# Optimization experiments

Measured on AMD Instinct MI355X. Metric: run time of the kernel, lower is better.

The kernel has to match this reference:

```python
import jax, jax.numpy as jnp
import numpy as np

B, T, IN, H, OUT = 512, 2048, 32, 256, 1
DT = 0.1
EPS = 1e-5


def setup_inputs() -> dict:
    key = jax.random.key(0)
    ks = jax.random.split(key, 16)
    n = lambda k, s, sc: jax.random.normal(k, s, jnp.float32) * sc
    d = {}
    d["x"] = n(ks[0], (B, T, IN), 1.0)
    d["Win0"] = n(ks[1], (IN, H), IN ** -0.5); d["bin0"] = jnp.zeros(H, jnp.float32)
    d["Wrec0"] = n(ks[2], (H, H), H ** -0.5); d["brec0"] = jnp.zeros(H, jnp.float32)
    d["Wattn0"] = n(ks[3], (H, H), H ** -0.5); d["battn0"] = jnp.zeros(H, jnp.float32)
    d["Wev0"] = n(ks[4], (2 * IN, 1), (2 * IN) ** -0.5); d["bev0"] = jnp.zeros(1, jnp.float32)
    d["tau0"] = jnp.ones(H, jnp.float32)
    d["gamma0"] = jnp.ones(H, jnp.float32); d["beta0"] = jnp.zeros(H, jnp.float32)
    d["Win1"] = n(ks[5], (H, H), H ** -0.5); d["bin1"] = jnp.zeros(H, jnp.float32)
    d["Wrec1"] = n(ks[6], (H, H), H ** -0.5); d["brec1"] = jnp.zeros(H, jnp.float32)
    d["Wattn1"] = n(ks[7], (H, H), H ** -0.5); d["battn1"] = jnp.zeros(H, jnp.float32)
    d["Wev1"] = n(ks[8], (2 * H, 1), (2 * H) ** -0.5); d["bev1"] = jnp.zeros(1, jnp.float32)
    d["tau1"] = jnp.ones(H, jnp.float32)
    d["gamma1"] = jnp.ones(H, jnp.float32); d["beta1"] = jnp.zeros(H, jnp.float32)
    d["Wskip"] = n(ks[9], (H, H), H ** -0.5); d["bskip"] = jnp.zeros(H, jnp.float32)
    d["Wout"] = n(ks[10], (H, OUT), H ** -0.5); d["bout"] = jnp.zeros(OUT, jnp.float32)
    return d


def _cell(xt, h, prev, mask, Win, bin_, Wrec, brec, Wattn, battn, Wev, bev, tau):
    # event weight from current and previous (detached) input; masked to 0 at t==0
    ew = jax.nn.sigmoid(jnp.concatenate([xt, prev], axis=1) @ Wev + bev) * mask  # [B,1]
    inp = jnp.tanh(xt @ Win + bin_)
    attn = jax.nn.sigmoid(h @ Wattn + battn)
    rec = jnp.tanh((h * attn) @ Wrec + brec)
    tau_c = jnp.clip(tau, 0.1, 10.0)
    new_h = h + DT * ((-h + inp + rec) / tau_c) * (1.0 + ew)
    return new_h, ew


def _ln(h, g, b):
    mu = h.mean(-1, keepdims=True)
    v = ((h - mu) ** 2).mean(-1, keepdims=True)
    return (h - mu) * jax.lax.rsqrt(v + EPS) * g + b


def _forward(x, Win0, bin0, Wrec0, brec0, Wattn0, battn0, Wev0, bev0, tau0, gamma0, beta0,
             Win1, bin1, Wrec1, brec1, Wattn1, battn1, Wev1, bev1, tau1, gamma1, beta1,
             Wskip, bskip, Wout, bout):
    Bv, Tv, _ = x.shape

    def step(carry, xs):
        h0, h1, p0, p1 = carry
        xt, mask = xs  # xt [B,IN], mask scalar-ish [1,1]
        h0n, ew0 = _cell(xt, h0, p0, mask, Win0, bin0, Wrec0, brec0, Wattn0, battn0, Wev0, bev0, tau0)
        h0n = _ln(h0n, gamma0, beta0)
        # layer 1 consumes the freshly updated layer-0 hidden (matches inner-loop order)
        h1n, ew1 = _cell(h0n, h1, p1, mask, Win1, bin1, Wrec1, brec1, Wattn1, battn1, Wev1, bev1, tau1)
        h1n = _ln(h1n, gamma1, beta1) + h0n @ Wskip + bskip
        new_carry = (h0n, h1n, jax.lax.stop_gradient(xt), jax.lax.stop_gradient(h0n))
        return new_carry, (ew0[:, 0], ew1[:, 0])

    xT = jnp.swapaxes(x, 0, 1)  # [T,B,IN]
    mask = (jnp.arange(Tv) > 0).astype(x.dtype)[:, None, None]  # [T,1,1]
    init = (jnp.zeros((Bv, H), x.dtype), jnp.zeros((Bv, H), x.dtype),
            jnp.zeros((Bv, x.shape[-1]), x.dtype), jnp.zeros((Bv, H), x.dtype))
    (h0, h1, _, _), (ew0s, ew1s) = jax.lax.scan(step, init, (xT, mask))
    out = h1 @ Wout + bout  # [B,OUT]
    return out, jnp.swapaxes(ew0s, 0, 1), jnp.swapaxes(ew1s, 0, 1)  # event weights [B,T]


def reference(x, Win0, bin0, Wrec0, brec0, Wattn0, battn0, Wev0, bev0, tau0, gamma0, beta0,
              Win1, bin1, Wrec1, brec1, Wattn1, battn1, Wev1, bev1, tau1, gamma1, beta1,
              Wskip, bskip, Wout, bout):
    return _forward(x, Win0, bin0, Wrec0, brec0, Wattn0, battn0, Wev0, bev0, tau0, gamma0, beta0,
                    Win1, bin1, Wrec1, brec1, Wattn1, battn1, Wev1, bev1, tau1, gamma1, beta1,
                    Wskip, bskip, Wout, bout)
```

## Files before the change

kernel.cpp:

```cpp
#include <hip/hip_runtime.h>
#include <math.h>

#define Bsz 512
#define Tsz 2048
#define INsz 32
#define Hsz 256

typedef __attribute__((ext_vector_type(8))) _Float16 half8;
typedef __attribute__((ext_vector_type(4))) float f32x4;

__device__ __forceinline__ f32x4 mfma16h(half8 a, half8 b, f32x4 c) {
    return __builtin_amdgcn_mfma_f32_16x16x32_f16(a, b, c, 0, 0, 0);
}
__device__ __forceinline__ float fsigmoid(float x) { return 1.0f / (1.0f + __expf(-x)); }
__device__ __forceinline__ float ftanh(float x) {
    float e = __expf(-2.0f * fabsf(x));
    float r = (1.0f - e) / (1.0f + e);
    return copysignf(r, x);
}

__global__ void ew0k(const float* __restrict__ x, const float* __restrict__ Wev0,
                     const float* __restrict__ bev0, float* __restrict__ ew0p) {
    int idx = blockIdx.x * 256 + threadIdx.x;
    int t = idx & (Tsz - 1);
    float e = 0.0f;
    if (t > 0) {
        const float* xc = x + (size_t)idx * INsz;
        const float* xp = xc - INsz;
        float acc = bev0[0];
#pragma unroll
        for (int k = 0; k < INsz; ++k) acc += xc[k] * Wev0[k] + xp[k] * Wev0[INsz + k];
        e = fsigmoid(acc);
    }
    ew0p[idx] = e;
}

__global__ void prep_frag(const float* __restrict__ W, _Float16* __restrict__ dst, int KC) {
    int tile = blockIdx.x / KC, kc = blockIdx.x % KC;
    int lane = threadIdx.x;
    int n16 = lane & 15, q = lane >> 4;
#pragma unroll
    for (int j = 0; j < 8; ++j) {
        int k = kc * 32 + q * 8 + j;
        float wv = W[(size_t)k * Hsz + tile * 16 + n16];
        _Float16 hi = (_Float16)wv;
        _Float16 lo = (_Float16)(wv - (float)hi);
        size_t rec = ((size_t)tile * KC + kc) * 2;
        dst[(rec + 0) * 512 + lane * 8 + j] = hi;
        dst[(rec + 1) * 512 + lane * 8 + j] = lo;
    }
}

__global__ __launch_bounds__(512, 2) void fused(
    const float* __restrict__ x, const float* __restrict__ ew0p, float* __restrict__ ew1p,
    const _Float16* __restrict__ fA0, const _Float16* __restrict__ fR0, const _Float16* __restrict__ fI0,
    const _Float16* __restrict__ fA1, const _Float16* __restrict__ fR1,
    const _Float16* __restrict__ fI1, const _Float16* __restrict__ fS1,
    const float* __restrict__ bin0, const float* __restrict__ brec0, const float* __restrict__ battn0,
    const float* __restrict__ tau0, const float* __restrict__ gamma0, const float* __restrict__ beta0,
    const float* __restrict__ bin1, const float* __restrict__ brec1, const float* __restrict__ battn1,
    const float* __restrict__ tau1, const float* __restrict__ gamma1, const float* __restrict__ beta1,
    const float* __restrict__ bskip, const float* __restrict__ Wev1, const float* __restrict__ bev1,
    _Float16* __restrict__ h0nA, _Float16* __restrict__ h0nB,
    float* __restrict__ in1bA, float* __restrict__ in1bB,
    float* __restrict__ skpbA, float* __restrict__ skpbB,
    float* __restrict__ h1s, int C, int L, int nch) {

    __shared__ _Float16 sAh[4096], sAl[4096];
    __shared__ _Float16 sW[65536];
    __shared__ float red[16][8][2];

    const int tid = threadIdx.x;
    const int w = tid >> 6, lane = tid & 63;
    const int n16 = lane & 15, q = lane >> 4;
    const int bx = blockIdx.x;

    if (bx < 32) {
        const int ci = L;
        if (ci >= nch) return;
        _Float16* __restrict__ h0n = (ci & 1) ? h0nB : h0nA;
        const _Float16* __restrict__ h0prev = (ci & 1) ? h0nA : h0nB;
        const int t0 = ci * C;
        const int rb = bx;
        const int r0 = rb * 16;
        const int c0 = w * 16 + n16, c1 = c0 + 128;

        for (int i = tid; i < 8192; i += 512) {
            int rec = i >> 6, off = i & 63;
            ((int4*)sW)[i] = ((const int4*)(fA0 + (size_t)rec * 2 * 512))[off];
        }
        half8 rB[2][8][2];
#pragma unroll
        for (int t2 = 0; t2 < 2; ++t2) {
            const int tile = t2 ? w + 8 : w;
#pragma unroll
            for (int kc = 0; kc < 8; ++kc) {
#pragma unroll
                for (int sp = 0; sp < 2; ++sp)
                    rB[t2][kc][sp] = *(const half8*)(fR0 + (((size_t)tile * 8 + kc) * 2 + sp) * 512 + lane * 8);
            }
        }
        half8 iB[2][2];
#pragma unroll
        for (int t2 = 0; t2 < 2; ++t2) {
            const int tile = t2 ? w + 8 : w;
#pragma unroll
            for (int sp = 0; sp < 2; ++sp)
                iB[t2][sp] = *(const half8*)(fI0 + ((size_t)tile * 2 + sp) * 512 + lane * 8);
        }
        float cbi[2], cbr[2], cba[2], ctau[2], cg[2], cb[2];
#pragma unroll
        for (int t2 = 0; t2 < 2; ++t2) {
            const int col = t2 ? c1 : c0;
            cbi[t2] = bin0[col]; cbr[t2] = brec0[col]; cba[t2] = battn0[col];
            ctau[t2] = 0.1f / fminf(fmaxf(tau0[col], 0.1f), 10.0f);
            cg[t2] = gamma0[col]; cb[t2] = beta0[col];
        }
        {
            const int4* src = (const int4*)(h0prev + ((size_t)C * 32 + rb) * 8192);
            int4 vh = src[tid], vl = src[tid + 512];
            ((int4*)sAh)[tid] = vh; ((int4*)sAl)[tid] = vl;
            int4* dst0 = (int4*)(h0n + (size_t)rb * 8192);
            dst0[tid] = vh; dst0[tid + 512] = vl;
        }
        __syncthreads();
        float h0reg[2][4];
#pragma unroll
        for (int t2 = 0; t2 < 2; ++t2) {
            const int col = t2 ? c1 : c0;
#pragma unroll
            for (int r = 0; r < 4; ++r) {
                int idx = ((col >> 3) * 16 + (q * 4 + r)) * 8 + (col & 7);
                h0reg[t2][r] = (float)sAh[idx] + (float)sAl[idx];
            }
        }
        auto pw = [&](int row, int col, float v) {
            int idx = ((col >> 3) * 16 + row) * 8 + (col & 7);
            _Float16 h = (_Float16)v;
            sAh[idx] = h;
            sAl[idx] = (_Float16)(v - (float)h);
        };

        const float* xbase = x + (size_t)(r0 + n16) * Tsz * INsz;
        const _Float16* lo0 = fA0 + ((size_t)w * 8 * 2 + 1) * 512 + lane * 8;
        const _Float16* lo1 = fA0 + (((size_t)(w + 8) * 8) * 2 + 1) * 512 + lane * 8;

        float4 xv0 = *(const float4*)(xbase + (size_t)t0 * INsz + q * 8);
        float4 xv1 = *(const float4*)(xbase + (size_t)t0 * INsz + q * 8 + 4);

#pragma unroll 1
        for (int s = 0; s < C; ++s) {
            const int t = t0 + s;
            float e0r[4];
#pragma unroll
            for (int r = 0; r < 4; ++r)
                e0r[r] = ew0p[(size_t)(r0 + q * 4 + r) * Tsz + t];
            half8 xh, xl;
            {
                float xv[8] = {xv0.x, xv0.y, xv0.z, xv0.w, xv1.x, xv1.y, xv1.z, xv1.w};
#pragma unroll
                for (int j = 0; j < 8; ++j) {
                    _Float16 h = (_Float16)xv[j];
                    xh[j] = h;
                    xl[j] = (_Float16)(xv[j] - (float)h);
                }
            }
            if (s + 1 < C) {
                const float* xp = xbase + (size_t)(t + 1) * INsz + q * 8;
                xv0 = *(const float4*)xp;
                xv1 = *(const float4*)(xp + 4);
            }
            f32x4 aA0 = {0,0,0,0}, aA1 = {0,0,0,0};
            {
                half8 nl0 = *(const half8*)(lo0);
                half8 nl1 = *(const half8*)(lo1);
#pragma unroll
                for (int kc = 0; kc < 8; ++kc) {
                    half8 cl0 = nl0, cl1 = nl1;
                    if (kc < 7) {
                        nl0 = *(const half8*)(lo0 + (size_t)(kc + 1) * 2 * 512);
                        nl1 = *(const half8*)(lo1 + (size_t)(kc + 1) * 2 * 512);
                    }
                    half8 ah = *(const half8*)&sAh[((kc * 4 + q) * 16 + n16) * 8];
                    half8 al = *(const half8*)&sAl[((kc * 4 + q) * 16 + n16) * 8];
                    half8 bh0 = *(const half8*)&sW[((w * 8 + kc) * 512) + lane * 8];
                    half8 bh1 = *(const half8*)&sW[(((w + 8) * 8 + kc) * 512) + lane * 8];
                    aA0 = mfma16h(ah, bh0, aA0); aA1 = mfma16h(ah, bh1, aA1);
                    aA0 = mfma16h(al, bh0, aA0); aA1 = mfma16h(al, bh1, aA1);
                    aA0 = mfma16h(ah, cl0, aA0); aA1 = mfma16h(ah, cl1, aA1);
                    aA0 = mfma16h(al, cl0, aA0); aA1 = mfma16h(al, cl1, aA1);
                }
            }
            f32x4 aI0 = {0,0,0,0}, aI1 = {0,0,0,0};
            aI0 = mfma16h(xh, iB[0][0], aI0); aI1 = mfma16h(xh, iB[1][0], aI1);
            aI0 = mfma16h(xl, iB[0][0], aI0); aI1 = mfma16h(xl, iB[1][0], aI1);
            aI0 = mfma16h(xh, iB[0][1], aI0); aI1 = mfma16h(xh, iB[1][1], aI1);
            aI0 = mfma16h(xl, iB[0][1], aI0); aI1 = mfma16h(xl, iB[1][1], aI1);
            __syncthreads();
#pragma unroll
            for (int r = 0; r < 4; ++r) {
                const int row = q * 4 + r;
                pw(row, c0, h0reg[0][r] * fsigmoid(aA0[r] + cba[0]));
                pw(row, c1, h0reg[1][r] * fsigmoid(aA1[r] + cba[1]));
            }
            __syncthreads();
            f32x4 aR0 = {0,0,0,0}, aR1 = {0,0,0,0};
#pragma unroll
            for (int kc = 0; kc < 8; ++kc) {
                half8 ah = *(const half8*)&sAh[((kc * 4 + q) * 16 + n16) * 8];
                half8 al = *(const half8*)&sAl[((kc * 4 + q) * 16 + n16) * 8];
                aR0 = mfma16h(ah, rB[0][kc][0], aR0); aR1 = mfma16h(ah, rB[1][kc][0], aR1);
                aR0 = mfma16h(al, rB[0][kc][0], aR0); aR1 = mfma16h(al, rB[1][kc][0], aR1);
                aR0 = mfma16h(ah, rB[0][kc][1], aR0); aR1 = mfma16h(ah, rB[1][kc][1], aR1);
                aR0 = mfma16h(al, rB[0][kc][1], aR0); aR1 = mfma16h(al, rB[1][kc][1], aR1);
            }
            float cell[2][4];
#pragma unroll
            for (int r = 0; r < 4; ++r) {
                float i0 = ftanh(aI0[r] + cbi[0]);
                float i1 = ftanh(aI1[r] + cbi[1]);
                float g0 = ftanh(aR0[r] + cbr[0]);
                float g1 = ftanh(aR1[r] + cbr[1]);
                float ef = 1.0f + e0r[r];
                cell[0][r] = h0reg[0][r] + ctau[0] * ef * (i0 + g0 - h0reg[0][r]);
                cell[1][r] = h0reg[1][r] + ctau[1] * ef * (i1 + g1 - h0reg[1][r]);
            }
#pragma unroll
            for (int r = 0; r < 4; ++r) {
                float pr = cell[0][r] + cell[1][r];
                float p2 = cell[0][r] * cell[0][r] + cell[1][r] * cell[1][r];
#pragma unroll
                for (int off = 1; off < 16; off <<= 1) {
                    pr += __shfl_xor(pr, off, 64);
                    p2 += __shfl_xor(p2, off, 64);
                }
                if (n16 == 0) { red[q * 4 + r][w][0] = pr; red[q * 4 + r][w][1] = p2; }
            }
            __syncthreads();
            float lnm[4], lnr[4];
#pragma unroll
            for (int r = 0; r < 4; ++r) {
                const int row = q * 4 + r;
                float S = 0.0f, Q2 = 0.0f;
#pragma unroll
                for (int wv = 0; wv < 8; ++wv) { S += red[row][wv][0]; Q2 += red[row][wv][1]; }
                float mu = S * (1.0f / 256.0f);
                float var = Q2 * (1.0f / 256.0f) - mu * mu;
                lnm[r] = mu;
                lnr[r] = 1.0f / sqrtf(var + 1e-5f);
            }
#pragma unroll
            for (int r = 0; r < 4; ++r) {
                const int row = q * 4 + r;
                float h0v = (cell[0][r] - lnm[r]) * lnr[r] * cg[0] + cb[0];
                float h1v = (cell[1][r] - lnm[r]) * lnr[r] * cg[1] + cb[1];
                pw(row, c0, h0v); pw(row, c1, h1v);
                h0reg[0][r] = h0v; h0reg[1][r] = h1v;
            }
            __syncthreads();
            int4* d = (int4*)(h0n + ((size_t)(s + 1) * 32 + rb) * 8192);
            d[tid] = ((const int4*)sAh)[tid];
            d[tid + 512] = ((const int4*)sAl)[tid];
        }
    } else if (bx < 64) {
        const int ci = L - 2;
        if (ci < 0) return;
        const float* __restrict__ in1b = (ci & 1) ? in1bB : in1bA;
        const float* __restrict__ skpb = (ci & 1) ? skpbB : skpbA;
        const int t0 = ci * C;
        const int rb = bx - 32;
        const int r0 = rb * 16;
        const int c0 = w * 16 + n16, c1 = c0 + 128;

        for (int i = tid; i < 8192; i += 512) {
            int rec = i >> 6, off = i & 63;
            ((int4*)sW)[i] = ((const int4*)(fA1 + (size_t)rec * 2 * 512))[off];
        }
        half8 rB[2][8][2];
#pragma unroll
        for (int t2 = 0; t2 < 2; ++t2) {
            const int tile = t2 ? w + 8 : w;
#pragma unroll
            for (int kc = 0; kc < 8; ++kc) {
#pragma unroll
                for (int sp = 0; sp < 2; ++sp)
                    rB[t2][kc][sp] = *(const half8*)(fR1 + (((size_t)tile * 8 + kc) * 2 + sp) * 512 + lane * 8);
            }
        }
        float cbr[2], cba[2], ctau[2], cg[2], cb[2];
#pragma unroll
        for (int t2 = 0; t2 < 2; ++t2) {
            const int col = t2 ? c1 : c0;
            cbr[t2] = brec1[col]; cba[t2] = battn1[col];
            ctau[t2] = 0.1f / fminf(fmaxf(tau1[col], 0.1f), 10.0f);
            cg[t2] = gamma1[col]; cb[t2] = beta1[col];
        }
        float h1reg[2][4];
#pragma unroll
        for (int t2 = 0; t2 < 2; ++t2) {
            const int col = t2 ? c1 : c0;
#pragma unroll
            for (int r = 0; r < 4; ++r) {
                const int row = q * 4 + r;
                float hv = h1s[(size_t)(r0 + row) * Hsz + col];
                h1reg[t2][r] = hv;
                int idx = ((col >> 3) * 16 + row) * 8 + (col & 7);
                _Float16 h = (_Float16)hv;
                sAh[idx] = h;
                sAl[idx] = (_Float16)(hv - (float)h);
            }
        }
        __syncthreads();

        auto pw = [&](int row, int col, float v) {
            int idx = ((col >> 3) * 16 + row) * 8 + (col & 7);
            _Float16 h = (_Float16)v;
            sAh[idx] = h;
            sAl[idx] = (_Float16)(v - (float)h);
        };
        const _Float16* lo0 = fA1 + ((size_t)w * 8 * 2 + 1) * 512 + lane * 8;
        const _Float16* lo1 = fA1 + (((size_t)(w + 8) * 8) * 2 + 1) * 512 + lane * 8;

#pragma unroll 1
        for (int s = 0; s < C; ++s) {
            const int t = t0 + s;
            float iv[2][4], sv[2][4], e1r[4];
#pragma unroll
            for (int r = 0; r < 4; ++r) {
                const int row = q * 4 + r;
                size_t i0 = ((size_t)s * Bsz + r0 + row) * Hsz + c0;
                size_t i1 = ((size_t)s * Bsz + r0 + row) * Hsz + c1;
                iv[0][r] = in1b[i0]; iv[1][r] = in1b[i1];
                sv[0][r] = skpb[i0]; sv[1][r] = skpb[i1];
                e1r[r] = ew1p[(size_t)(r0 + row) * Tsz + t];
            }
            f32x4 aA0 = {0,0,0,0}, aA1 = {0,0,0,0};
            {
                half8 nl0 = *(const half8*)(lo0);
                half8 nl1 = *(const half8*)(lo1);
#pragma unroll
                for (int kc = 0; kc < 8; ++kc) {
                    half8 cl0 = nl0, cl1 = nl1;
                    if (kc < 7) {
                        nl0 = *(const half8*)(lo0 + (size_t)(kc + 1) * 2 * 512);
                        nl1 = *(const half8*)(lo1 + (size_t)(kc + 1) * 2 * 512);
                    }
                    half8 ah = *(const half8*)&sAh[((kc * 4 + q) * 16 + n16) * 8];
                    half8 al = *(const half8*)&sAl[((kc * 4 + q) * 16 + n16) * 8];
                    half8 bh0 = *(const half8*)&sW[((w * 8 + kc) * 512) + lane * 8];
                    half8 bh1 = *(const half8*)&sW[(((w + 8) * 8 + kc) * 512) + lane * 8];
                    aA0 = mfma16h(ah, bh0, aA0); aA1 = mfma16h(ah, bh1, aA1);
                    aA0 = mfma16h(al, bh0, aA0); aA1 = mfma16h(al, bh1, aA1);
                    aA0 = mfma16h(ah, cl0, aA0); aA1 = mfma16h(ah, cl1, aA1);
                    aA0 = mfma16h(al, cl0, aA0); aA1 = mfma16h(al, cl1, aA1);
                }
            }
            __syncthreads();
#pragma unroll
            for (int r = 0; r < 4; ++r) {
                const int row = q * 4 + r;
                pw(row, c0, h1reg[0][r] * fsigmoid(aA0[r] + cba[0]));
                pw(row, c1, h1reg[1][r] * fsigmoid(aA1[r] + cba[1]));
            }
            __syncthreads();
            f32x4 aR0 = {0,0,0,0}, aR1 = {0,0,0,0};
#pragma unroll
            for (int kc = 0; kc < 8; ++kc) {
                half8 ah = *(const half8*)&sAh[((kc * 4 + q) * 16 + n16) * 8];
                half8 al = *(const half8*)&sAl[((kc * 4 + q) * 16 + n16) * 8];
                aR0 = mfma16h(ah, rB[0][kc][0], aR0); aR1 = mfma16h(ah, rB[1][kc][0], aR1);
                aR0 = mfma16h(al, rB[0][kc][0], aR0); aR1 = mfma16h(al, rB[1][kc][0], aR1);
                aR0 = mfma16h(ah, rB[0][kc][1], aR0); aR1 = mfma16h(ah, rB[1][kc][1], aR1);
                aR0 = mfma16h(al, rB[0][kc][1], aR0); aR1 = mfma16h(al, rB[1][kc][1], aR1);
            }
            float cell[2][4];
#pragma unroll
            for (int r = 0; r < 4; ++r) {
                float g0 = ftanh(aR0[r] + cbr[0]);
                float g1 = ftanh(aR1[r] + cbr[1]);
                float ef = 1.0f + e1r[r];
                cell[0][r] = h1reg[0][r] + ctau[0] * ef * (iv[0][r] + g0 - h1reg[0][r]);
                cell[1][r] = h1reg[1][r] + ctau[1] * ef * (iv[1][r] + g1 - h1reg[1][r]);
            }
#pragma unroll
            for (int r = 0; r < 4; ++r) {
                float pr = cell[0][r] + cell[1][r];
                float p2 = cell[0][r] * cell[0][r] + cell[1][r] * cell[1][r];
#pragma unroll
                for (int off = 1; off < 16; off <<= 1) {
                    pr += __shfl_xor(pr, off, 64);
                    p2 += __shfl_xor(p2, off, 64);
                }
                if (n16 == 0) { red[q * 4 + r][w][0] = pr; red[q * 4 + r][w][1] = p2; }
            }
            __syncthreads();
            float lnm[4], lnr[4];
#pragma unroll
            for (int r = 0; r < 4; ++r) {
                const int row = q * 4 + r;
                float S = 0.0f, Q2 = 0.0f;
#pragma unroll
                for (int wv = 0; wv < 8; ++wv) { S += red[row][wv][0]; Q2 += red[row][wv][1]; }
                float mu = S * (1.0f / 256.0f);
                float var = Q2 * (1.0f / 256.0f) - mu * mu;
                lnm[r] = mu;
                lnr[r] = 1.0f / sqrtf(var + 1e-5f);
            }
#pragma unroll
            for (int r = 0; r < 4; ++r) {
                const int row = q * 4 + r;
                float h0v = (cell[0][r] - lnm[r]) * lnr[r] * cg[0] + cb[0] + sv[0][r];
                float h1v = (cell[1][r] - lnm[r]) * lnr[r] * cg[1] + cb[1] + sv[1][r];
                pw(row, c0, h0v); pw(row, c1, h1v);
                h1reg[0][r] = h0v; h1reg[1][r] = h1v;
            }
            __syncthreads();
        }
#pragma unroll
        for (int t2 = 0; t2 < 2; ++t2) {
            const int col = t2 ? c1 : c0;
#pragma unroll
            for (int r = 0; r < 4; ++r)
                h1s[(size_t)(r0 + q * 4 + r) * Hsz + col] = h1reg[t2][r];
        }
    } else if (bx < 64 + C * 4) {
        const int ci = L - 1;
        if (ci < 0 || ci >= nch) return;
        const _Float16* __restrict__ h0n = (ci & 1) ? h0nB : h0nA;
        float* __restrict__ in1b = (ci & 1) ? in1bB : in1bA;
        float* __restrict__ skpb = (ci & 1) ? skpbB : skpbA;
        const int bi = bx - 64;
        const int sbase = (bi >> 5) * 8;
        const int rb = bi & 31;
        const int r0 = rb * 16;
        const int c0 = w * 16 + n16, c1 = c0 + 128;
        float cbi[2], cbs[2];
#pragma unroll
        for (int t2 = 0; t2 < 2; ++t2) {
            const int col = t2 ? c1 : c0;
            cbi[t2] = bin1[col]; cbs[t2] = bskip[col];
        }
        for (int i = 0; i < 8; ++i) {
            const int s = sbase + i;
            const _Float16* abase = h0n + ((size_t)(s + 1) * 32 + rb) * 8192;
            f32x4 aI0 = {0,0,0,0}, aI1 = {0,0,0,0}, aS0 = {0,0,0,0}, aS1 = {0,0,0,0};
#pragma unroll
            for (int kc = 0; kc < 8; ++kc) {
                half8 ah = *(const half8*)&abase[((kc * 4 + q) * 16 + n16) * 8];
                half8 al = *(const half8*)&abase[4096 + ((kc * 4 + q) * 16 + n16) * 8];
                size_t o0 = (((size_t)w * 8 + kc) * 2) * 512 + lane * 8;
                size_t o1 = (((size_t)(w + 8) * 8 + kc) * 2) * 512 + lane * 8;
                half8 bh0 = *(const half8*)(fI1 + o0), bl0 = *(const half8*)(fI1 + o0 + 512);
                half8 bh1 = *(const half8*)(fI1 + o1), bl1 = *(const half8*)(fI1 + o1 + 512);
                aI0 = mfma16h(ah, bh0, aI0); aI1 = mfma16h(ah, bh1, aI1);
                aI0 = mfma16h(al, bh0, aI0); aI1 = mfma16h(al, bh1, aI1);
                aI0 = mfma16h(ah, bl0, aI0); aI1 = mfma16h(ah, bl1, aI1);
                aI0 = mfma16h(al, bl0, aI0); aI1 = mfma16h(al, bl1, aI1);
                half8 ch0 = *(const half8*)(fS1 + o0), cl0 = *(const half8*)(fS1 + o0 + 512);
                half8 ch1 = *(const half8*)(fS1 + o1), cl1 = *(const half8*)(fS1 + o1 + 512);
                aS0 = mfma16h(ah, ch0, aS0); aS1 = mfma16h(ah, ch1, aS1);
                aS0 = mfma16h(al, ch0, aS0); aS1 = mfma16h(al, ch1, aS1);
                aS0 = mfma16h(ah, cl0, aS0); aS1 = mfma16h(ah, cl1, aS1);
                aS0 = mfma16h(al, cl0, aS0); aS1 = mfma16h(al, cl1, aS1);
            }
#pragma unroll
            for (int r = 0; r < 4; ++r) {
                const int row = q * 4 + r;
                size_t i0 = ((size_t)s * Bsz + r0 + row) * Hsz + c0;
                size_t i1 = ((size_t)s * Bsz + r0 + row) * Hsz + c1;
                in1b[i0] = ftanh(aI0[r] + cbi[0]);
                in1b[i1] = ftanh(aI1[r] + cbi[1]);
                skpb[i0] = aS0[r] + cbs[0];
                skpb[i1] = aS1[r] + cbs[1];
            }
        }
    } else {
        const int ci = L - 1;
        if (ci < 0 || ci >= nch) return;
        const _Float16* __restrict__ h0n = (ci & 1) ? h0nB : h0nA;
        const int t0 = ci * C;
        const int bi = bx - 64 - C * 4;
        const int wid = bi * 8 + w;
        const int s = wid >> 5, rb = wid & 31;
        float acc = 0.0f;
#pragma unroll
        for (int half = 0; half < 2; ++half) {
            const _Float16* base = h0n + ((size_t)(half ? s : s + 1) * 32 + rb) * 8192;
#pragma unroll
            for (int kc = 0; kc < 8; ++kc) {
                half8 ah = *(const half8*)&base[((kc * 4 + q) * 16 + n16) * 8];
                half8 al = *(const half8*)&base[4096 + ((kc * 4 + q) * 16 + n16) * 8];
                const float* wv = Wev1 + half * 256 + kc * 32 + q * 8;
#pragma unroll
                for (int j = 0; j < 8; ++j)
                    acc += ((float)ah[j] + (float)al[j]) * wv[j];
            }
        }
        acc += __shfl_xor(acc, 16, 64);
        acc += __shfl_xor(acc, 32, 64);
        const int t = t0 + s;
        if (q == 0) {
            float e = (t > 0) ? fsigmoid(acc + bev1[0]) : 0.0f;
            ew1p[(size_t)(rb * 16 + n16) * Tsz + t] = e;
        }
    }
}

__global__ void outk(const float* __restrict__ h1s, const float* __restrict__ Wout,
                     const float* __restrict__ bout, float* __restrict__ outp) {
    const int w = threadIdx.x >> 6, lane = threadIdx.x & 63;
    const int b = blockIdx.x * 4 + w;
    float4 hv = *(const float4*)(h1s + (size_t)b * Hsz + lane * 4);
    float4 wv = *(const float4*)(Wout + lane * 4);
    float acc = hv.x * wv.x + hv.y * wv.y + hv.z * wv.z + hv.w * wv.w;
#pragma unroll
    for (int off = 1; off < 64; off <<= 1) acc += __shfl_xor(acc, off, 64);
    if (lane == 0) outp[b] = acc + bout[0];
}

extern "C" void kernel_launch(void* const* d_in, const int* in_sizes, int n_in,
                              void* d_out, int out_size, void* d_ws, size_t ws_size,
                              hipStream_t stream) {
    const float* x      = (const float*)d_in[0];
    const float* Win0   = (const float*)d_in[1];
    const float* bin0   = (const float*)d_in[2];
    const float* Wrec0  = (const float*)d_in[3];
    const float* brec0  = (const float*)d_in[4];
    const float* Wattn0 = (const float*)d_in[5];
    const float* battn0 = (const float*)d_in[6];
    const float* Wev0   = (const float*)d_in[7];
    const float* bev0   = (const float*)d_in[8];
    const float* tau0   = (const float*)d_in[9];
    const float* gamma0 = (const float*)d_in[10];
    const float* beta0  = (const float*)d_in[11];
    const float* Win1   = (const float*)d_in[12];
    const float* bin1   = (const float*)d_in[13];
    const float* Wrec1  = (const float*)d_in[14];
    const float* brec1  = (const float*)d_in[15];
    const float* Wattn1 = (const float*)d_in[16];
    const float* battn1 = (const float*)d_in[17];
    const float* Wev1   = (const float*)d_in[18];
    const float* bev1   = (const float*)d_in[19];
    const float* tau1   = (const float*)d_in[20];
    const float* gamma1 = (const float*)d_in[21];
    const float* beta1  = (const float*)d_in[22];
    const float* Wskip  = (const float*)d_in[23];
    const float* bskip  = (const float*)d_in[24];
    const float* Wout   = (const float*)d_in[25];
    const float* bout   = (const float*)d_in[26];

    float* outp = (float*)d_out;
    float* ew0p = outp + Bsz;
    float* ew1p = ew0p + (size_t)Bsz * Tsz;

    _Float16* p = (_Float16*)d_ws;
    _Float16* fA0 = p; p += 131072;
    _Float16* fR0 = p; p += 131072;
    _Float16* fA1 = p; p += 131072;
    _Float16* fR1 = p; p += 131072;
    _Float16* fI1 = p; p += 131072;
    _Float16* fS1 = p; p += 131072;
    _Float16* fI0 = p; p += 16384;
    size_t frag_bytes = (size_t)(6 * 131072 + 16384) * 2;

    int C = 128;
    while (C > 16) {
        size_t need = frag_bytes
                    + 2 * ((size_t)(C + 1) * 524288)
                    + 4 * ((size_t)C * 524288)
                    + 524288;
        if (need <= ws_size) break;
        C >>= 1;
    }
    char* qp = (char*)d_ws + frag_bytes;
    _Float16* h0nA = (_Float16*)qp; qp += (size_t)(C + 1) * 524288;
    _Float16* h0nB = (_Float16*)qp; qp += (size_t)(C + 1) * 524288;
    float* in1bA = (float*)qp;      qp += (size_t)C * 524288;
    float* in1bB = (float*)qp;      qp += (size_t)C * 524288;
    float* skpbA = (float*)qp;      qp += (size_t)C * 524288;
    float* skpbB = (float*)qp;      qp += (size_t)C * 524288;
    float* h1s = (float*)qp;
    (void)in_sizes; (void)n_in; (void)out_size;

    hipMemsetAsync(h0nB + (size_t)C * 32 * 8192, 0, 524288, stream);
    hipMemsetAsync(h1s, 0, 524288, stream);

    ew0k<<<(Bsz * Tsz) / 256, 256, 0, stream>>>(x, Wev0, bev0, ew0p);
    prep_frag<<<16 * 8, 64, 0, stream>>>(Wattn0, fA0, 8);
    prep_frag<<<16 * 8, 64, 0, stream>>>(Wrec0,  fR0, 8);
    prep_frag<<<16 * 8, 64, 0, stream>>>(Wattn1, fA1, 8);
    prep_frag<<<16 * 8, 64, 0, stream>>>(Wrec1,  fR1, 8);
    prep_frag<<<16 * 8, 64, 0, stream>>>(Win1,   fI1, 8);
    prep_frag<<<16 * 8, 64, 0, stream>>>(Wskip,  fS1, 8);
    prep_frag<<<16 * 1, 64, 0, stream>>>(Win0,   fI0, 1);

    const int nch = Tsz / C;
    const int grid = 64 + C * 8;
    for (int L = 0; L < nch + 2; ++L) {
        fused<<<grid, 512, 0, stream>>>(
            x, ew0p, ew1p, fA0, fR0, fI0, fA1, fR1, fI1, fS1,
            bin0, brec0, battn0, tau0, gamma0, beta0,
            bin1, brec1, battn1, tau1, gamma1, beta1,
            bskip, Wev1, bev1,
            h0nA, h0nB, in1bA, in1bB, skpbA, skpbB, h1s, C, L, nch);
    }
    outk<<<Bsz / 4, 256, 0, stream>>>(h1s, Wout, bout, outp);
}
```

Before: 23.04 ms.

## Double-buffer gated state in LDS to drop a barrier; halve LDS weights; shrink chunk

Adds a separate LDS buffer for the attention-gated hidden state, so the gate write no longer overwrites the hidden-state tile still being read. That removes one __syncthreads per timestep in both recurrent layers. To make room, only half of the attention weights stay in LDS, and the second column tile's high part is streamed from global memory with register prefetch. It also prefetches the next step's event weight early and halves the chunk size C, which trades more launches and more global weight traffic for less barrier overhead.

```diff
diff --git a/kernel.cpp b/kernel.cpp
--- a/kernel.cpp
+++ b/kernel.cpp
@@ -67,7 +67,8 @@
     float* __restrict__ h1s, int C, int L, int nch) {
 
     __shared__ _Float16 sAh[4096], sAl[4096];
-    __shared__ _Float16 sW[65536];
+    __shared__ _Float16 sGh[4096], sGl[4096];
+    __shared__ _Float16 sW[32768];
     __shared__ float red[16][8][2];
 
     const int tid = threadIdx.x;
@@ -85,7 +86,7 @@
         const int r0 = rb * 16;
         const int c0 = w * 16 + n16, c1 = c0 + 128;
 
-        for (int i = tid; i < 8192; i += 512) {
+        for (int i = tid; i < 4096; i += 512) {
             int rec = i >> 6, off = i & 63;
             ((int4*)sW)[i] = ((const int4*)(fA0 + (size_t)rec * 2 * 512))[off];
         }
@@ -134,27 +135,34 @@
                 h0reg[t2][r] = (float)sAh[idx] + (float)sAl[idx];
             }
         }
-        auto pw = [&](int row, int col, float v) {
+        auto pwA = [&](int row, int col, float v) {
             int idx = ((col >> 3) * 16 + row) * 8 + (col & 7);
             _Float16 h = (_Float16)v;
             sAh[idx] = h;
             sAl[idx] = (_Float16)(v - (float)h);
         };
+        auto pwG = [&](int row, int col, float v) {
+            int idx = ((col >> 3) * 16 + row) * 8 + (col & 7);
+            _Float16 h = (_Float16)v;
+            sGh[idx] = h;
+            sGl[idx] = (_Float16)(v - (float)h);
+        };
 
         const float* xbase = x + (size_t)(r0 + n16) * Tsz * INsz;
         const _Float16* lo0 = fA0 + ((size_t)w * 8 * 2 + 1) * 512 + lane * 8;
-        const _Float16* lo1 = fA0 + (((size_t)(w + 8) * 8) * 2 + 1) * 512 + lane * 8;
+        const _Float16* hi1 = fA0 + ((size_t)(w + 8) * 8 * 2 + 0) * 512 + lane * 8;
+        const _Float16* lo1 = fA0 + ((size_t)(w + 8) * 8 * 2 + 1) * 512 + lane * 8;
 
         float4 xv0 = *(const float4*)(xbase + (size_t)t0 * INsz + q * 8);
         float4 xv1 = *(const float4*)(xbase + (size_t)t0 * INsz + q * 8 + 4);
+        float e0r[4];
+#pragma unroll
+        for (int r = 0; r < 4; ++r)
+            e0r[r] = ew0p[(size_t)(r0 + q * 4 + r) * Tsz + t0];
 
 #pragma unroll 1
         for (int s = 0; s < C; ++s) {
             const int t = t0 + s;
-            float e0r[4];
-#pragma unroll
-            for (int r = 0; r < 4; ++r)
-                e0r[r] = ew0p[(size_t)(r0 + q * 4 + r) * Tsz + t];
             half8 xh, xl;
             {
                 float xv[8] = {xv0.x, xv0.y, xv0.z, xv0.w, xv1.x, xv1.y, xv1.z, xv1.w};
@@ -173,20 +181,21 @@
             f32x4 aA0 = {0,0,0,0}, aA1 = {0,0,0,0};
             {
                 half8 nl0 = *(const half8*)(lo0);
+                half8 nh1 = *(const half8*)(hi1);
                 half8 nl1 = *(const half8*)(lo1);
 #pragma unroll
                 for (int kc = 0; kc < 8; ++kc) {
-                    half8 cl0 = nl0, cl1 = nl1;
+                    half8 cl0 = nl0, ch1 = nh1, cl1 = nl1;
                     if (kc < 7) {
                         nl0 = *(const half8*)(lo0 + (size_t)(kc + 1) * 2 * 512);
+                        nh1 = *(const half8*)(hi1 + (size_t)(kc + 1) * 2 * 512);
                         nl1 = *(const half8*)(lo1 + (size_t)(kc + 1) * 2 * 512);
                     }
                     half8 ah = *(const half8*)&sAh[((kc * 4 + q) * 16 + n16) * 8];
                     half8 al = *(const half8*)&sAl[((kc * 4 + q) * 16 + n16) * 8];
                     half8 bh0 = *(const half8*)&sW[((w * 8 + kc) * 512) + lane * 8];
-                    half8 bh1 = *(const half8*)&sW[(((w + 8) * 8 + kc) * 512) + lane * 8];
-                    aA0 = mfma16h(ah, bh0, aA0); aA1 = mfma16h(ah, bh1, aA1);
-                    aA0 = mfma16h(al, bh0, aA0); aA1 = mfma16h(al, bh1, aA1);
+                    aA0 = mfma16h(ah, bh0, aA0); aA1 = mfma16h(ah, ch1, aA1);
+                    aA0 = mfma16h(al, bh0, aA0); aA1 = mfma16h(al, ch1, aA1);
                     aA0 = mfma16h(ah, cl0, aA0); aA1 = mfma16h(ah, cl1, aA1);
                     aA0 = mfma16h(al, cl0, aA0); aA1 = mfma16h(al, cl1, aA1);
                 }
@@ -196,19 +205,18 @@
             aI0 = mfma16h(xl, iB[0][0], aI0); aI1 = mfma16h(xl, iB[1][0], aI1);
             aI0 = mfma16h(xh, iB[0][1], aI0); aI1 = mfma16h(xh, iB[1][1], aI1);
             aI0 = mfma16h(xl, iB[0][1], aI0); aI1 = mfma16h(xl, iB[1][1], aI1);
-            __syncthreads();
-#pragma unroll
-            for (int r = 0; r < 4; ++r) {
-                const int row = q * 4 + r;
-                pw(row, c0, h0reg[0][r] * fsigmoid(aA0[r] + cba[0]));
-                pw(row, c1, h0reg[1][r] * fsigmoid(aA1[r] + cba[1]));
+#pragma unroll
+            for (int r = 0; r < 4; ++r) {
+                const int row = q * 4 + r;
+                pwG(row, c0, h0reg[0][r] * fsigmoid(aA0[r] + cba[0]));
+                pwG(row, c1, h0reg[1][r] * fsigmoid(aA1[r] + cba[1]));
             }
             __syncthreads();
             f32x4 aR0 = {0,0,0,0}, aR1 = {0,0,0,0};
 #pragma unroll
             for (int kc = 0; kc < 8; ++kc) {
-                half8 ah = *(const half8*)&sAh[((kc * 4 + q) * 16 + n16) * 8];
-                half8 al = *(const half8*)&sAl[((kc * 4 + q) * 16 + n16) * 8];
+                half8 ah = *(const half8*)&sGh[((kc * 4 + q) * 16 + n16) * 8];
+                half8 al = *(const half8*)&sGl[((kc * 4 + q) * 16 + n16) * 8];
                 aR0 = mfma16h(ah, rB[0][kc][0], aR0); aR1 = mfma16h(ah, rB[1][kc][0], aR1);
                 aR0 = mfma16h(al, rB[0][kc][0], aR0); aR1 = mfma16h(al, rB[1][kc][0], aR1);
                 aR0 = mfma16h(ah, rB[0][kc][1], aR0); aR1 = mfma16h(ah, rB[1][kc][1], aR1);
@@ -225,6 +233,11 @@
                 cell[0][r] = h0reg[0][r] + ctau[0] * ef * (i0 + g0 - h0reg[0][r]);
                 cell[1][r] = h0reg[1][r] + ctau[1] * ef * (i1 + g1 - h0reg[1][r]);
             }
+            if (s + 1 < C) {
+#pragma unroll
+                for (int r = 0; r < 4; ++r)
+                    e0r[r] = ew0p[(size_t)(r0 + q * 4 + r) * Tsz + t + 1];
+            }
 #pragma unroll
             for (int r = 0; r < 4; ++r) {
                 float pr = cell[0][r] + cell[1][r];
@@ -254,7 +267,7 @@
                 const int row = q * 4 + r;
                 float h0v = (cell[0][r] - lnm[r]) * lnr[r] * cg[0] + cb[0];
                 float h1v = (cell[1][r] - lnm[r]) * lnr[r] * cg[1] + cb[1];
-                pw(row, c0, h0v); pw(row, c1, h1v);
+                pwA(row, c0, h0v); pwA(row, c1, h1v);
                 h0reg[0][r] = h0v; h0reg[1][r] = h1v;
             }
             __syncthreads();
@@ -272,7 +285,7 @@
         const int r0 = rb * 16;
         const int c0 = w * 16 + n16, c1 = c0 + 128;
 
-        for (int i = tid; i < 8192; i += 512) {
+        for (int i = tid; i < 4096; i += 512) {
             int rec = i >> 6, off = i & 63;
             ((int4*)sW)[i] = ((const int4*)(fA1 + (size_t)rec * 2 * 512))[off];
         }
@@ -312,19 +325,31 @@
         }
         __syncthreads();
 
-        auto pw = [&](int row, int col, float v) {
+        auto pwA = [&](int row, int col, float v) {
             int idx = ((col >> 3) * 16 + row) * 8 + (col & 7);
             _Float16 h = (_Float16)v;
             sAh[idx] = h;
             sAl[idx] = (_Float16)(v - (float)h);
         };
+        auto pwG = [&](int row, int col, float v) {
+            int idx = ((col >> 3) * 16 + row) * 8 + (col & 7);
+            _Float16 h = (_Float16)v;
+            sGh[idx] = h;
+            sGl[idx] = (_Float16)(v - (float)h);
+        };
         const _Float16* lo0 = fA1 + ((size_t)w * 8 * 2 + 1) * 512 + lane * 8;
-        const _Float16* lo1 = fA1 + (((size_t)(w + 8) * 8) * 2 + 1) * 512 + lane * 8;
+        const _Float16* hi1 = fA1 + ((size_t)(w + 8) * 8 * 2 + 0) * 512 + lane * 8;
+        const _Float16* lo1 = fA1 + ((size_t)(w + 8) * 8 * 2 + 1) * 512 + lane * 8;
+
+        float e1r[4];
+#pragma unroll
+        for (int r = 0; r < 4; ++r)
+            e1r[r] = ew1p[(size_t)(r0 + q * 4 + r) * Tsz + t0];
 
 #pragma unroll 1
         for (int s = 0; s < C; ++s) {
             const int t = t0 + s;
-            float iv[2][4], sv[2][4], e1r[4];
+            float iv[2][4], sv[2][4];
 #pragma unroll
             for (int r = 0; r < 4; ++r) {
                 const int row = q * 4 + r;
@@ -332,42 +357,41 @@
                 size_t i1 = ((size_t)s * Bsz + r0 + row) * Hsz + c1;
                 iv[0][r] = in1b[i0]; iv[1][r] = in1b[i1];
                 sv[0][r] = skpb[i0]; sv[1][r] = skpb[i1];
-                e1r[r] = ew1p[(size_t)(r0 + row) * Tsz + t];
             }
             f32x4 aA0 = {0,0,0,0}, aA1 = {0,0,0,0};
             {
                 half8 nl0 = *(const half8*)(lo0);
+                half8 nh1 = *(const half8*)(hi1);
                 half8 nl1 = *(const half8*)(lo1);
 #pragma unroll
                 for (int kc = 0; kc < 8; ++kc) {
-                    half8 cl0 = nl0, cl1 = nl1;
+                    half8 cl0 = nl0, ch1 = nh1, cl1 = nl1;
                     if (kc < 7) {
                         nl0 = *(const half8*)(lo0 + (size_t)(kc + 1) * 2 * 512);
+                        nh1 = *(const half8*)(hi1 + (size_t)(kc + 1) * 2 * 512);
                         nl1 = *(const half8*)(lo1 + (size_t)(kc + 1) * 2 * 512);
                     }
                     half8 ah = *(const half8*)&sAh[((kc * 4 + q) * 16 + n16) * 8];
                     half8 al = *(const half8*)&sAl[((kc * 4 + q) * 16 + n16) * 8];
                     half8 bh0 = *(const half8*)&sW[((w * 8 + kc) * 512) + lane * 8];
-                    half8 bh1 = *(const half8*)&sW[(((w + 8) * 8 + kc) * 512) + lane * 8];
-                    aA0 = mfma16h(ah, bh0, aA0); aA1 = mfma16h(ah, bh1, aA1);
-                    aA0 = mfma16h(al, bh0, aA0); aA1 = mfma16h(al, bh1, aA1);
+                    aA0 = mfma16h(ah, bh0, aA0); aA1 = mfma16h(ah, ch1, aA1);
+                    aA0 = mfma16h(al, bh0, aA0); aA1 = mfma16h(al, ch1, aA1);
                     aA0 = mfma16h(ah, cl0, aA0); aA1 = mfma16h(ah, cl1, aA1);
                     aA0 = mfma16h(al, cl0, aA0); aA1 = mfma16h(al, cl1, aA1);
                 }
             }
-            __syncthreads();
-#pragma unroll
-            for (int r = 0; r < 4; ++r) {
-                const int row = q * 4 + r;
-                pw(row, c0, h1reg[0][r] * fsigmoid(aA0[r] + cba[0]));
-                pw(row, c1, h1reg[1][r] * fsigmoid(aA1[r] + cba[1]));
+#pragma unroll
+            for (int r = 0; r < 4; ++r) {
+                const int row = q * 4 + r;
+                pwG(row, c0, h1reg[0][r] * fsigmoid(aA0[r] + cba[0]));
+                pwG(row, c1, h1reg[1][r] * fsigmoid(aA1[r] + cba[1]));
             }
             __syncthreads();
             f32x4 aR0 = {0,0,0,0}, aR1 = {0,0,0,0};
 #pragma unroll
             for (int kc = 0; kc < 8; ++kc) {
-                half8 ah = *(const half8*)&sAh[((kc * 4 + q) * 16 + n16) * 8];
-                half8 al = *(const half8*)&sAl[((kc * 4 + q) * 16 + n16) * 8];
+                half8 ah = *(const half8*)&sGh[((kc * 4 + q) * 16 + n16) * 8];
+                half8 al = *(const half8*)&sGl[((kc * 4 + q) * 16 + n16) * 8];
                 aR0 = mfma16h(ah, rB[0][kc][0], aR0); aR1 = mfma16h(ah, rB[1][kc][0], aR1);
                 aR0 = mfma16h(al, rB[0][kc][0], aR0); aR1 = mfma16h(al, rB[1][kc][0], aR1);
                 aR0 = mfma16h(ah, rB[0][kc][1], aR0); aR1 = mfma16h(ah, rB[1][kc][1], aR1);
@@ -382,6 +406,11 @@
                 cell[0][r] = h1reg[0][r] + ctau[0] * ef * (iv[0][r] + g0 - h1reg[0][r]);
                 cell[1][r] = h1reg[1][r] + ctau[1] * ef * (iv[1][r] + g1 - h1reg[1][r]);
             }
+            if (s + 1 < C) {
+#pragma unroll
+                for (int r = 0; r < 4; ++r)
+                    e1r[r] = ew1p[(size_t)(r0 + q * 4 + r) * Tsz + t + 1];
+            }
 #pragma unroll
             for (int r = 0; r < 4; ++r) {
                 float pr = cell[0][r] + cell[1][r];
@@ -411,7 +440,7 @@
                 const int row = q * 4 + r;
                 float h0v = (cell[0][r] - lnm[r]) * lnr[r] * cg[0] + cb[0] + sv[0][r];
                 float h1v = (cell[1][r] - lnm[r]) * lnr[r] * cg[1] + cb[1] + sv[1][r];
-                pw(row, c0, h0v); pw(row, c1, h1v);
+                pwA(row, c0, h0v); pwA(row, c1, h1v);
                 h1reg[0][r] = h0v; h1reg[1][r] = h1v;
             }
             __syncthreads();
@@ -563,7 +592,7 @@
     _Float16* fI0 = p; p += 16384;
     size_t frag_bytes = (size_t)(6 * 131072 + 16384) * 2;
 
-    int C = 128;
+    int C = 64;
     while (C > 16) {
         size_t need = frag_bytes
                     + 2 * ((size_t)(C + 1) * 524288)
```

After: 29.25 ms. +27.0%, slower.
